# Kernel tuning notes

Measured on AMD Instinct MI355X. Metric: run time of the kernel, lower is better.

## Reference

```python
import jax, jax.numpy as jnp
import numpy as np


def _per_batch_terms(logits, target, X1, Y1, X2, Y2, T):
    # logits: [B, C]; target: [B]; X1/X2: [1, C] float; Y1/Y2: [1, C] int; T: [1] float
    B = logits.shape[0]
    rows = jnp.arange(B)
    lsm = jax.nn.log_softmax(logits, axis=-1)          # stable exp(x)/sum(exp(x))
    p_t = jnp.exp(lsm[rows, target])                    # [B] target prob
    y1 = Y1[0, target]                                  # [B] correlated class 1
    y2 = Y2[0, target]                                  # [B] correlated class 2
    x1 = X1[0, target]
    x2 = X2[0, target]
    P1 = jnp.exp(lsm[rows, y1])
    P2 = jnp.exp(lsm[rows, y2])
    t = T[0]
    corr = t * (x1 * P1 + x2 * P2)                      # [B]
    cond = p_t > corr
    safe_diff = jnp.where(cond, p_t - corr, 1.0)
    loss_i = jnp.where(cond, -jnp.log(safe_diff), -jnp.log(p_t))
    nz = jnp.logical_or(P1 != 0.0, P2 != 0.0)
    k_mask = jnp.logical_and(cond, nz)
    safe_corr = jnp.where(k_mask, corr, 1.0)
    z_i = jnp.where(k_mask, p_t / safe_corr, 0.0)
    k_i = k_mask.astype(logits.dtype)
    j_i = (~cond).astype(logits.dtype)
    return loss_i, k_i, z_i, j_i


def setup_inputs() -> dict:
    key = jax.random.key(0)
    k1, k2, k3, k4, k5, k6 = jax.random.split(key, 6)
    B, C = 4096, 32000
    inp = {
        "input": jax.random.normal(k1, (B, C), dtype=jnp.float32),
        "target": jax.random.randint(k2, (B,), 0, C, dtype=jnp.int64),
        "X1": jax.random.uniform(k3, (1, C), dtype=jnp.float32),
        "Y1": jax.random.randint(k4, (1, C), 0, C, dtype=jnp.int64),
        "X2": jax.random.uniform(k5, (1, C), dtype=jnp.float32),
        "Y2": jax.random.randint(k6, (1, C), 0, C, dtype=jnp.int64),
        "T": jnp.full((1,), 0.5, dtype=jnp.float32),
    }
    return inp


def reference(input, target, X1, Y1, X2, Y2, T):
    loss_i, k_i, z_i, j_i = _per_batch_terms(input, target, X1, Y1, X2, Y2, T)
    B = input.shape[0]
    batch_loss = jnp.sum(loss_i) / B  # size_average=True
    return (batch_loss, jnp.sum(k_i), jnp.sum(z_i), jnp.sum(j_i))
```

## Files before the change

### kernel.cpp

```cpp
#include <hip/hip_runtime.h>
#include <math.h>

#define BLOCK 256

__global__ __launch_bounds__(BLOCK) void ccel_kernel(
    const float* __restrict__ input,
    const int*   __restrict__ target,
    const float* __restrict__ X1,
    const int*   __restrict__ Y1,
    const float* __restrict__ X2,
    const int*   __restrict__ Y2,
    const float* __restrict__ T,
    float* __restrict__ out,
    int C, float invB)
{
    const int row = blockIdx.x;
    const int tid = threadIdx.x;
    const float* __restrict__ rowp = input + (size_t)row * (size_t)C;
    const float4* __restrict__ rp4 = reinterpret_cast<const float4*>(rowp);
    const int n4 = C >> 2;

    float s0 = 0.f, s1 = 0.f, s2 = 0.f, s3 = 0.f;
    float s4 = 0.f, s5 = 0.f, s6 = 0.f, s7 = 0.f;

    int i = tid;
    for (; i + BLOCK < n4; i += 2 * BLOCK) {
        float4 a = rp4[i];
        float4 b = rp4[i + BLOCK];
        s0 += __expf(a.x); s1 += __expf(a.y);
        s2 += __expf(a.z); s3 += __expf(a.w);
        s4 += __expf(b.x); s5 += __expf(b.y);
        s6 += __expf(b.z); s7 += __expf(b.w);
    }
    if (i < n4) {
        float4 a = rp4[i];
        s0 += __expf(a.x); s1 += __expf(a.y);
        s2 += __expf(a.z); s3 += __expf(a.w);
    }
    for (int j = (n4 << 2) + tid; j < C; j += BLOCK) s0 += __expf(rowp[j]);

    float s = ((s0 + s1) + (s2 + s3)) + ((s4 + s5) + (s6 + s7));

    #pragma unroll
    for (int off = 32; off > 0; off >>= 1)
        s += __shfl_down(s, off, 64);

    __shared__ float warp_s[BLOCK / 64];
    const int wave = tid >> 6;
    const int lane = tid & 63;
    if (lane == 0) warp_s[wave] = s;
    __syncthreads();

    if (tid == 0) {
        float S = warp_s[0];
        #pragma unroll
        for (int w = 1; w < BLOCK / 64; ++w) S += warp_s[w];

        const float logZ = logf(S);
        const int   t  = target[row];
        const float xt = rowp[t];
        const int   y1 = Y1[t];
        const int   y2 = Y2[t];
        const float x1 = X1[t];
        const float x2 = X2[t];
        const float P1 = expf(rowp[y1] - logZ);
        const float P2 = expf(rowp[y2] - logZ);
        const float pt = expf(xt - logZ);
        const float corr = T[0] * (x1 * P1 + x2 * P2);
        const bool cond = pt > corr;
        const float loss = cond ? -logf(pt - corr) : -logf(pt);
        const bool nz = (P1 != 0.f) || (P2 != 0.f);
        const bool k = cond && nz;
        const float z = k ? (pt / corr) : 0.f;
        atomicAdd(out + 0, loss * invB);
        atomicAdd(out + 1, k ? 1.f : 0.f);
        atomicAdd(out + 2, z);
        atomicAdd(out + 3, cond ? 0.f : 1.f);
    }
}

extern "C" void kernel_launch(void* const* d_in, const int* in_sizes, int n_in,
                              void* d_out, int out_size, void* d_ws, size_t ws_size,
                              hipStream_t stream) {
    const float* input  = (const float*)d_in[0];
    const int*   target = (const int*)  d_in[1];
    const float* X1     = (const float*)d_in[2];
    const int*   Y1     = (const int*)  d_in[3];
    const float* X2     = (const float*)d_in[4];
    const int*   Y2     = (const int*)  d_in[5];
    const float* T      = (const float*)d_in[6];
    float* out = (float*)d_out;

    const int B = in_sizes[1];
    const int C = in_sizes[2];

    hipMemsetAsync(out, 0, (size_t)out_size * sizeof(float), stream);

    ccel_kernel<<<dim3(B), dim3(BLOCK), 0, stream>>>(
        input, target, X1, Y1, X2, Y2, T, out, C, 1.0f / (float)B);
}
```

Before: 811.3 us.

## Split row sum into chunked wave sweep kernel plus separate loss kernel

Replaces the one-block-per-row kernel with a persistent grid of wavefronts. Each wavefront processes fixed 1280-float chunks using nontemporal vector loads and atomically adds partial exp-sums into a per-row workspace. A second kernel computes the per-row loss terms with one thread per row and reduces them per wave before the atomics. This targets load imbalance and low memory-level parallelism, and drops the serial per-block tail. In exchange it adds an extra launch, a workspace memset, per-chunk atomics and 64-bit division in the loop index math.

Result: faster. 658.8 us (-18.8%).

```diff
diff --git a/kernel.cpp b/kernel.cpp
--- a/kernel.cpp
+++ b/kernel.cpp
@@ -2,8 +2,55 @@
 #include <math.h>
 
 #define BLOCK 256
+#define CHUNK_FLOATS 1280
+#define SWEEP_BLOCKS 2048
 
-__global__ __launch_bounds__(BLOCK) void ccel_kernel(
+typedef float f4_t __attribute__((ext_vector_type(4)));
+
+__global__ __launch_bounds__(BLOCK) void sum_kernel(
+    const float* __restrict__ input,
+    float* __restrict__ ws,
+    int B, int C)
+{
+    const int lane = threadIdx.x & 63;
+    const int wid  = (blockIdx.x * BLOCK + threadIdx.x) >> 6;
+    const int nw   = (gridDim.x * BLOCK) >> 6;
+    const int cpr  = (C + CHUNK_FLOATS - 1) / CHUNK_FLOATS;
+    const long long K = (long long)B * cpr;
+    const f4_t* __restrict__ in4 = reinterpret_cast<const f4_t*>(input);
+    const int n4 = C >> 2;
+    const bool c4 = (C & 3) == 0;
+
+    for (long long k = wid; k < K; k += nw) {
+        const int row = (int)(k / cpr);
+        const int c   = (int)(k - (long long)row * cpr);
+        float acc;
+        if (c4 && (c + 1) * CHUNK_FLOATS <= C) {
+            const long long base = (long long)row * n4 + (long long)c * (CHUNK_FLOATS / 4) + lane;
+            f4_t v0 = __builtin_nontemporal_load(&in4[base]);
+            f4_t v1 = __builtin_nontemporal_load(&in4[base + 64]);
+            f4_t v2 = __builtin_nontemporal_load(&in4[base + 128]);
+            f4_t v3 = __builtin_nontemporal_load(&in4[base + 192]);
+            f4_t v4 = __builtin_nontemporal_load(&in4[base + 256]);
+            float t0 = __expf(v0.x) + __expf(v1.x) + __expf(v2.x) + __expf(v3.x) + __expf(v4.x);
+            float t1 = __expf(v0.y) + __expf(v1.y) + __expf(v2.y) + __expf(v3.y) + __expf(v4.y);
+            float t2 = __expf(v0.z) + __expf(v1.z) + __expf(v2.z) + __expf(v3.z) + __expf(v4.z);
+            float t3 = __expf(v0.w) + __expf(v1.w) + __expf(v2.w) + __expf(v3.w) + __expf(v4.w);
+            acc = (t0 + t1) + (t2 + t3);
+        } else {
+            acc = 0.f;
+            const float* __restrict__ rp = input + (size_t)row * (size_t)C;
+            for (int j = c * CHUNK_FLOATS + lane; j < C; j += 64)
+                acc += __expf(rp[j]);
+        }
+        #pragma unroll
+        for (int off = 32; off > 0; off >>= 1)
+            acc += __shfl_down(acc, off, 64);
+        if (lane == 0) atomicAdd(ws + row, acc);
+    }
+}
+
+__global__ __launch_bounds__(BLOCK) void loss_kernel(
     const float* __restrict__ input,
     const int*   __restrict__ target,
     const float* __restrict__ X1,
@@ -11,71 +58,48 @@
     const float* __restrict__ X2,
     const int*   __restrict__ Y2,
     const float* __restrict__ T,
+    const float* __restrict__ ws,
     float* __restrict__ out,
-    int C, float invB)
+    int B, int C, float invB)
 {
-    const int row = blockIdx.x;
-    const int tid = threadIdx.x;
-    const float* __restrict__ rowp = input + (size_t)row * (size_t)C;
-    const float4* __restrict__ rp4 = reinterpret_cast<const float4*>(rowp);
-    const int n4 = C >> 2;
-
-    float s0 = 0.f, s1 = 0.f, s2 = 0.f, s3 = 0.f;
-    float s4 = 0.f, s5 = 0.f, s6 = 0.f, s7 = 0.f;
-
-    int i = tid;
-    for (; i + BLOCK < n4; i += 2 * BLOCK) {
-        float4 a = rp4[i];
-        float4 b = rp4[i + BLOCK];
-        s0 += __expf(a.x); s1 += __expf(a.y);
-        s2 += __expf(a.z); s3 += __expf(a.w);
-        s4 += __expf(b.x); s5 += __expf(b.y);
-        s6 += __expf(b.z); s7 += __expf(b.w);
-    }
-    if (i < n4) {
-        float4 a = rp4[i];
-        s0 += __expf(a.x); s1 += __expf(a.y);
-        s2 += __expf(a.z); s3 += __expf(a.w);
-    }
-    for (int j = (n4 << 2) + tid; j < C; j += BLOCK) s0 += __expf(rowp[j]);
-
-    float s = ((s0 + s1) + (s2 + s3)) + ((s4 + s5) + (s6 + s7));
-
-    #pragma unroll
-    for (int off = 32; off > 0; off >>= 1)
-        s += __shfl_down(s, off, 64);
-
-    __shared__ float warp_s[BLOCK / 64];
-    const int wave = tid >> 6;
-    const int lane = tid & 63;
-    if (lane == 0) warp_s[wave] = s;
-    __syncthreads();
-
-    if (tid == 0) {
-        float S = warp_s[0];
-        #pragma unroll
-        for (int w = 1; w < BLOCK / 64; ++w) S += warp_s[w];
-
+    const int r = blockIdx.x * BLOCK + threadIdx.x;
+    float loss = 0.f, kf = 0.f, z = 0.f, jf = 0.f;
+    if (r < B) {
+        const float S = ws[r];
         const float logZ = logf(S);
-        const int   t  = target[row];
-        const float xt = rowp[t];
+        const float* __restrict__ rowp = input + (size_t)r * (size_t)C;
+        const int   t  = target[r];
         const int   y1 = Y1[t];
         const int   y2 = Y2[t];
         const float x1 = X1[t];
         const float x2 = X2[t];
-        const float P1 = expf(rowp[y1] - logZ);
-        const float P2 = expf(rowp[y2] - logZ);
+        const float xt = rowp[t];
+        const float r1 = rowp[y1];
+        const float r2 = rowp[y2];
+        const float P1 = expf(r1 - logZ);
+        const float P2 = expf(r2 - logZ);
         const float pt = expf(xt - logZ);
         const float corr = T[0] * (x1 * P1 + x2 * P2);
         const bool cond = pt > corr;
-        const float loss = cond ? -logf(pt - corr) : -logf(pt);
+        loss = (cond ? -logf(pt - corr) : -logf(pt)) * invB;
         const bool nz = (P1 != 0.f) || (P2 != 0.f);
         const bool k = cond && nz;
-        const float z = k ? (pt / corr) : 0.f;
-        atomicAdd(out + 0, loss * invB);
-        atomicAdd(out + 1, k ? 1.f : 0.f);
+        kf = k ? 1.f : 0.f;
+        z  = k ? (pt / corr) : 0.f;
+        jf = cond ? 0.f : 1.f;
+    }
+    #pragma unroll
+    for (int off = 32; off > 0; off >>= 1) {
+        loss += __shfl_down(loss, off, 64);
+        kf   += __shfl_down(kf,   off, 64);
+        z    += __shfl_down(z,    off, 64);
+        jf   += __shfl_down(jf,   off, 64);
+    }
+    if ((threadIdx.x & 63) == 0) {
+        atomicAdd(out + 0, loss);
+        atomicAdd(out + 1, kf);
         atomicAdd(out + 2, z);
-        atomicAdd(out + 3, cond ? 0.f : 1.f);
+        atomicAdd(out + 3, jf);
     }
 }
 
@@ -90,12 +114,15 @@
     const int*   Y2     = (const int*)  d_in[5];
     const float* T      = (const float*)d_in[6];
     float* out = (float*)d_out;
+    float* ws  = (float*)d_ws;
 
     const int B = in_sizes[1];
     const int C = in_sizes[2];
 
-    hipMemsetAsync(out, 0, (size_t)out_size * sizeof(float), stream);
+    (void)hipMemsetAsync(out, 0, (size_t)out_size * sizeof(float), stream);
+    (void)hipMemsetAsync(ws, 0, (size_t)B * sizeof(float), stream);
 
-    ccel_kernel<<<dim3(B), dim3(BLOCK), 0, stream>>>(
-        input, target, X1, Y1, X2, Y2, T, out, C, 1.0f / (float)B);
+    sum_kernel<<<dim3(SWEEP_BLOCKS), dim3(BLOCK), 0, stream>>>(input, ws, B, C);
+    loss_kernel<<<dim3((B + BLOCK - 1) / BLOCK), dim3(BLOCK), 0, stream>>>(
+        input, target, X1, Y1, X2, Y2, T, ws, out, B, C, 1.0f / (float)B);
 }
```
